# Kernel tuning notes

Measured on AMD Instinct MI355X. Metric: run time of the kernel, lower is better.

## Reference

```python
import jax, jax.numpy as jnp
import numpy as np

B, T, H, N = 4, 512, 32, 64
D = H * N  # n_embd = 2048


def setup_inputs() -> dict:
    key = jax.random.key(0)
    ks = jax.random.split(key, 8)
    f = lambda kk: jax.random.normal(kk, (B, T, H, N), dtype=jnp.float32)
    r = f(ks[0])
    w = f(ks[1])
    k = f(ks[2])
    v = f(ks[3])
    iclr = f(ks[4])
    # int8-style quantized output projection: int values in [-128,127] + per-row scale
    w_out_q = jax.random.randint(ks[5], (D, D), -128, 128, dtype=jnp.int32)
    w_out_scale = jax.random.uniform(ks[6], (D,), dtype=jnp.float32) * 0.01
    return {"r": r, "w": w, "k": k, "v": v, "iclr": iclr,
            "w_out_q": w_out_q, "w_out_scale": w_out_scale}


def _wkv7(r, w, k, v, iclr):
    """RWKV x070 WKV scan. All inputs [B,T,H,N]; returns [B,T,H*N]."""
    decay = jnp.exp(-jnp.exp(w))  # per-channel decay in (0,1), x070 parameterization
    # kk = l2-normalized key direction; a = -kk (removal), b = kk * sigmoid(iclr) (write)
    kk = k * jax.lax.rsqrt(jnp.sum(k * k, axis=-1, keepdims=True) + 1e-12)
    a = -kk
    b = kk * jax.nn.sigmoid(iclr)

    def step(state, inp):
        # state: [B,H,N,N]; each inp element: [B,H,N]
        r_t, d_t, k_t, v_t, a_t, b_t = inp
        sa = jnp.einsum('bhij,bhj->bhi', state, a_t)
        state = (state * d_t[:, :, None, :]
                 + sa[..., None] * b_t[:, :, None, :]
                 + v_t[..., None] * k_t[:, :, None, :])
        y_t = jnp.einsum('bhij,bhj->bhi', state, r_t)
        return state, y_t

    tb = lambda x: jnp.swapaxes(x, 0, 1)  # [B,T,H,N] -> [T,B,H,N]
    state0 = jnp.zeros((B, H, N, N), dtype=r.dtype)
    _, y = jax.lax.scan(step, state0, (tb(r), tb(decay), tb(k), tb(v), tb(a), tb(b)))
    return jnp.swapaxes(y, 0, 1).reshape(B, T, H * N)


def reference(r, w, k, v, iclr, w_out_q, w_out_scale):
    y = _wkv7(r, w, k, v, iclr)               # [B,T,D]
    # inline dequant of quantized output projection (per-output-row scale)
    W = w_out_q.astype(jnp.float32) * w_out_scale[:, None]  # [D,D]
    return jnp.einsum('btd,od->bto', y, W)    # [B,T,D]
```

## Files before the change

kernel.cpp:

```cpp
#include <hip/hip_runtime.h>
#include <hip/hip_bf16.h>
#include <stdint.h>

#define B_ 4
#define T_ 512
#define H_ 32
#define N_ 64
#define D_ 2048
#define M_ (B_*T_)

typedef __attribute__((ext_vector_type(4))) float f32x4;
typedef __attribute__((ext_vector_type(8))) short short8;

template <int CTRL>
__device__ __forceinline__ float dpp_add(float x) {
    int t = __builtin_amdgcn_mov_dpp(__float_as_int(x), CTRL, 0xF, 0xF, true);
    return x + __int_as_float(t);
}
__device__ __forceinline__ float bfly16(float x) {
    x = dpp_add<0xB1>(x);
    x = dpp_add<0x4E>(x);
    x = dpp_add<0x141>(x);
    x = dpp_add<0x140>(x);
    return x;
}

__device__ __forceinline__ void gld16(const float* g, float* l) {
    __builtin_amdgcn_global_load_lds(
        (const __attribute__((address_space(1))) unsigned int*)g,
        (__attribute__((address_space(3))) unsigned int*)l, 16, 0, 0);
}

__global__ __launch_bounds__(256) void prep(
    const float* __restrict__ r, const float* __restrict__ w,
    const float* __restrict__ k, const float* __restrict__ v,
    const float* __restrict__ iclr, float* __restrict__ pk) {
    int g = blockIdx.x * 4 + (threadIdx.x >> 6);
    int lane = threadIdx.x & 63;
    int b = g >> 14;
    int t = (g >> 5) & (T_ - 1);
    int h = g & 31;
    size_t si = (size_t)g * 64 + lane;
    size_t di = (((size_t)(b * H_ + h) * T_) + t) * 384 + lane;
    float rv = r[si], wv = w[si], kv = k[si], vv = v[si], av = iclr[si];
    float d = expf(-expf(wv));
    float ss = kv * kv;
#pragma unroll
    for (int m = 1; m < 64; m <<= 1) ss += __shfl_xor(ss, m, 64);
    float kkv = kv * rsqrtf(ss + 1e-12f);
    float bbv = kkv * (1.f / (1.f + expf(-av)));
    pk[di          ] = rv;
    pk[di + 1 * 64 ] = kv;
    pk[di + 2 * 64 ] = vv;
    pk[di + 3 * 64 ] = d;
    pk[di + 4 * 64 ] = kkv;
    pk[di + 5 * 64 ] = bbv;
}

__global__ __launch_bounds__(512) void wkv_scan(
    const float* __restrict__ pk, __hip_bfloat16* __restrict__ y,
    const int* __restrict__ q, __hip_bfloat16* __restrict__ o) {
    if (blockIdx.x >= 256) {
        int i = ((blockIdx.x - 256) * 512 + (int)threadIdx.x) * 4;
        int4 qi = *(const int4*)(q + i);
        __hip_bfloat16 t[4];
        t[0] = __float2bfloat16((float)qi.x);
        t[1] = __float2bfloat16((float)qi.y);
        t[2] = __float2bfloat16((float)qi.z);
        t[3] = __float2bfloat16((float)qi.w);
        *(uint2*)(o + i) = *(uint2*)t;
        return;
    }
    const int bh   = blockIdx.x & 127;
    const int half = blockIdx.x >> 7;
    const int tid  = threadIdx.x;
    const int wave = tid >> 6;
    const int lane = tid & 63;
    const int b = bh >> 5, h = bh & 31;
    const int jg = lane & 15;
    const int rl = lane >> 4;
    const int row = (half * 8 + wave) * 4 + rl;

    __shared__ __align__(16) float ring[2 * 1536];

    const float* src = pk + (size_t)bh * T_ * 384;

    if (wave == 0) {
#pragma unroll
        for (int gg = 0; gg < 2; ++gg)
#pragma unroll
            for (int c = 0; c < 6; ++c)
                gld16(src + gg * 1536 + c * 256 + lane * 4,
                      &ring[gg * 1536 + c * 256]);
    }

    float S[4] = {0.f, 0.f, 0.f, 0.f};

    for (int g = 0; g < T_ / 4; ++g) {
        if (wave == 0) {
            if (g == 0) { asm volatile("s_waitcnt vmcnt(6)"  ::: "memory"); }
            else        { asm volatile("s_waitcnt vmcnt(10)" ::: "memory"); }
        }
        asm volatile("s_barrier" ::: "memory");
        const float* rb0 = &ring[(g & 1) * 1536];

#pragma unroll
        for (int i = 0; i < 4; ++i) {
            const int t = g * 4 + i;
            const float* rb = rb0 + i * 384;

            f32x4 Rc = *(const f32x4*)(rb + 0 * 64 + jg * 4);
            f32x4 Kc = *(const f32x4*)(rb + 1 * 64 + jg * 4);
            float vcv =                 rb[2 * 64 + row];
            f32x4 Dc = *(const f32x4*)(rb + 3 * 64 + jg * 4);
            f32x4 Ac = *(const f32x4*)(rb + 4 * 64 + jg * 4);
            f32x4 Bc = *(const f32x4*)(rb + 5 * 64 + jg * 4);

            float s01 = fmaf(S[1], Ac[1], S[0] * Ac[0]);
            float s23 = fmaf(S[3], Ac[3], S[2] * Ac[2]);
            const float sa = -bfly16(s01 + s23);

            float t0 = fmaf(sa, Bc[0], vcv * Kc[0]);
            S[0] = fmaf(S[0], Dc[0], t0);
            float t1 = fmaf(sa, Bc[1], vcv * Kc[1]);
            S[1] = fmaf(S[1], Dc[1], t1);
            float y01 = fmaf(S[1], Rc[1], S[0] * Rc[0]);
            float t2 = fmaf(sa, Bc[2], vcv * Kc[2]);
            S[2] = fmaf(S[2], Dc[2], t2);
            float t3 = fmaf(sa, Bc[3], vcv * Kc[3]);
            S[3] = fmaf(S[3], Dc[3], t3);
            float y23 = fmaf(S[3], Rc[3], S[2] * Rc[2]);
            float ys = bfly16(y01 + y23);
            if (jg == 0)
                y[((size_t)b * T_ + t) * D_ + h * 64 + row] = __float2bfloat16(ys);
        }

        asm volatile("s_barrier" ::: "memory");

        if (wave == 0) {
            int gp = g + 2; if (gp > T_ / 4 - 1) gp = T_ / 4 - 1;
            const float* g0 = src + (size_t)gp * 1536 + lane * 4;
            float* l0 = &ring[(g & 1) * 1536];
#pragma unroll
            for (int c = 0; c < 6; ++c)
                gld16(g0 + c * 256, l0 + c * 256);
        }
    }
}

__device__ __forceinline__ void gload_lds16(const __hip_bfloat16* g, ushort* l) {
    __builtin_amdgcn_global_load_lds(
        (const __attribute__((address_space(1))) unsigned int*)g,
        (__attribute__((address_space(3))) unsigned int*)l, 16, 0, 0);
}

__global__ __launch_bounds__(256, 2) void gemm_bt(
    const __hip_bfloat16* __restrict__ A,
    const __hip_bfloat16* __restrict__ Bq,
    const float* __restrict__ scale,
    float* __restrict__ C) {
    const int K = D_;
    __shared__ __align__(16) ushort As[2][128 * 64];
    __shared__ __align__(16) ushort Bs[2][64 * 64];

    const int tid = threadIdx.x;
    const int lane = tid & 63;
    const int wave = tid >> 6;
    const int wr = wave >> 1, wc = wave & 1;

    const int id = blockIdx.x;
    const int swz = (id & 7) * 64 + (id >> 3);
    const int m0 = (swz & 15) * 128;
    const int n0 = (swz >> 4) * 64;

    const int srow8 = lane >> 3;
    const int scol8 = (lane & 7) * 8;
    const int ml = lane & 15;
    const int kq = (lane >> 4) * 8;

    f32x4 acc[4][2] = {};

#define GSTAGE(slot, kk0)                                                    \
    {                                                                        \
        _Pragma("unroll")                                                    \
        for (int c = 0; c < 4; ++c) {                                        \
            int ra = wave * 32 + c * 8;                                      \
            gload_lds16(A + (size_t)(m0 + ra + srow8) * K + (kk0) + scol8,   \
                        &As[slot][ra * 64]);                                 \
        }                                                                    \
        _Pragma("unroll")                                                    \
        for (int c = 0; c < 2; ++c) {                                        \
            int rb = wave * 16 + c * 8;                                      \
            gload_lds16(Bq + (size_t)(n0 + rb + srow8) * K + (kk0) + scol8,  \
                        &Bs[slot][rb * 64]);                                 \
        }                                                                    \
    }

    GSTAGE(0, 0);

    for (int t = 0; t < K / 64; ++t) {
        if (t + 1 < K / 64) {
            GSTAGE((t + 1) & 1, (t + 1) * 64);
            asm volatile("s_waitcnt vmcnt(6)" ::: "memory");
        } else {
            asm volatile("s_waitcnt vmcnt(0)" ::: "memory");
        }
        asm volatile("s_barrier" ::: "memory");
        const int sl = t & 1;
#pragma unroll
        for (int ks = 0; ks < 2; ++ks) {
            short8 af[4], bf[2];
#pragma unroll
            for (int tm = 0; tm < 4; ++tm)
                af[tm] = *(const short8*)(&As[sl][(wr * 64 + tm * 16 + ml) * 64 + ks * 32 + kq]);
#pragma unroll
            for (int tn = 0; tn < 2; ++tn)
                bf[tn] = *(const short8*)(&Bs[sl][(wc * 32 + tn * 16 + ml) * 64 + ks * 32 + kq]);
#pragma unroll
            for (int tm = 0; tm < 4; ++tm)
#pragma unroll
                for (int tn = 0; tn < 2; ++tn)
                    acc[tm][tn] = __builtin_amdgcn_mfma_f32_16x16x32_bf16(
                        af[tm], bf[tn], acc[tm][tn], 0, 0, 0);
        }
        asm volatile("s_barrier" ::: "memory");
    }
#undef GSTAGE

#pragma unroll
    for (int tn = 0; tn < 2; ++tn) {
        int gn = n0 + wc * 32 + tn * 16 + ml;
        float sc = scale[gn];
#pragma unroll
        for (int tm = 0; tm < 4; ++tm) {
            int gm = m0 + wr * 64 + tm * 16 + (lane >> 4) * 4;
#pragma unroll
            for (int rg = 0; rg < 4; ++rg)
                C[(size_t)(gm + rg) * D_ + gn] = acc[tm][tn][rg] * sc;
        }
    }
}

extern "C" void kernel_launch(void* const* d_in, const int* in_sizes, int n_in,
                              void* d_out, int out_size, void* d_ws, size_t ws_size,
                              hipStream_t stream) {
    (void)in_sizes; (void)n_in; (void)out_size; (void)ws_size;
    const float* r  = (const float*)d_in[0];
    const float* w  = (const float*)d_in[1];
    const float* k  = (const float*)d_in[2];
    const float* v  = (const float*)d_in[3];
    const float* ic = (const float*)d_in[4];
    const int*   wq = (const int*)d_in[5];
    const float* sc = (const float*)d_in[6];
    float* out = (float*)d_out;

    char* p = (char*)d_ws;
    __hip_bfloat16* yb = (__hip_bfloat16*)p;  p += (size_t)M_ * D_ * 2;
    __hip_bfloat16* wb = (__hip_bfloat16*)p;  p += (size_t)D_ * D_ * 2;
    float* pk = (float*)p;

    prep    <<<dim3(16384), dim3(256), 0, stream>>>(r, w, k, v, ic, pk);
    wkv_scan<<<dim3(256 + 2048), dim3(512), 0, stream>>>(pk, yb, wq, wb);
    gemm_bt <<<dim3(512), dim3(256), 0, stream>>>(yb, wb, sc, out);
}
```

Before: 287.8 us.

## Fuse prep into WKV scan and enlarge GEMM tile to 128x128

Removes the separate prep kernel and its packed workspace. The scan kernel now streams raw r/w/k/v/iclr rows into shared memory with 4-byte global-to-LDS loads and computes decay, normalized key and sigmoid gate inline using fast exp2/rcp/rsq intrinsics. This saves a kernel launch and a full write-then-read of the packed intermediate, but the serial scan loop now carries extra transcendental work and many more small load instructions. The GEMM also moves to 128x128 tiles with 256 blocks, which raises per-block reuse but halves the grid and drops the two-blocks-per-CU occupancy hint.

```diff
diff --git a/kernel.cpp b/kernel.cpp
--- a/kernel.cpp
+++ b/kernel.cpp
@@ -25,40 +25,16 @@
     return x;
 }
 
-__device__ __forceinline__ void gld16(const float* g, float* l) {
+__device__ __forceinline__ void gld4(const float* g, float* l) {
     __builtin_amdgcn_global_load_lds(
         (const __attribute__((address_space(1))) unsigned int*)g,
-        (__attribute__((address_space(3))) unsigned int*)l, 16, 0, 0);
-}
-
-__global__ __launch_bounds__(256) void prep(
+        (__attribute__((address_space(3))) unsigned int*)l, 4, 0, 0);
+}
+
+__global__ __launch_bounds__(512) void wkv_scan(
     const float* __restrict__ r, const float* __restrict__ w,
     const float* __restrict__ k, const float* __restrict__ v,
-    const float* __restrict__ iclr, float* __restrict__ pk) {
-    int g = blockIdx.x * 4 + (threadIdx.x >> 6);
-    int lane = threadIdx.x & 63;
-    int b = g >> 14;
-    int t = (g >> 5) & (T_ - 1);
-    int h = g & 31;
-    size_t si = (size_t)g * 64 + lane;
-    size_t di = (((size_t)(b * H_ + h) * T_) + t) * 384 + lane;
-    float rv = r[si], wv = w[si], kv = k[si], vv = v[si], av = iclr[si];
-    float d = expf(-expf(wv));
-    float ss = kv * kv;
-#pragma unroll
-    for (int m = 1; m < 64; m <<= 1) ss += __shfl_xor(ss, m, 64);
-    float kkv = kv * rsqrtf(ss + 1e-12f);
-    float bbv = kkv * (1.f / (1.f + expf(-av)));
-    pk[di          ] = rv;
-    pk[di + 1 * 64 ] = kv;
-    pk[di + 2 * 64 ] = vv;
-    pk[di + 3 * 64 ] = d;
-    pk[di + 4 * 64 ] = kkv;
-    pk[di + 5 * 64 ] = bbv;
-}
-
-__global__ __launch_bounds__(512) void wkv_scan(
-    const float* __restrict__ pk, __hip_bfloat16* __restrict__ y,
+    const float* __restrict__ iclr, __hip_bfloat16* __restrict__ y,
     const int* __restrict__ q, __hip_bfloat16* __restrict__ o) {
     if (blockIdx.x >= 256) {
         int i = ((blockIdx.x - 256) * 512 + (int)threadIdx.x) * 4;
@@ -81,40 +57,63 @@
     const int rl = lane >> 4;
     const int row = (half * 8 + wave) * 4 + rl;
 
-    __shared__ __align__(16) float ring[2 * 1536];
-
-    const float* src = pk + (size_t)bh * T_ * 384;
+    __shared__ __align__(16) float ring[2 * 1280];
+
+    const float L2E = 1.4426950408889634f;
 
     if (wave == 0) {
 #pragma unroll
         for (int gg = 0; gg < 2; ++gg)
 #pragma unroll
-            for (int c = 0; c < 6; ++c)
-                gld16(src + gg * 1536 + c * 256 + lane * 4,
-                      &ring[gg * 1536 + c * 256]);
+            for (int i = 0; i < 4; ++i) {
+                size_t base = ((size_t)(b * T_ + gg * 4 + i) * H_ + h) * 64 + lane;
+                float* l = &ring[gg * 1280 + i * 320];
+                gld4(r + base, l);
+                gld4(w + base, l + 64);
+                gld4(k + base, l + 128);
+                gld4(v + base, l + 192);
+                gld4(iclr + base, l + 256);
+            }
     }
 
     float S[4] = {0.f, 0.f, 0.f, 0.f};
 
     for (int g = 0; g < T_ / 4; ++g) {
         if (wave == 0) {
-            if (g == 0) { asm volatile("s_waitcnt vmcnt(6)"  ::: "memory"); }
-            else        { asm volatile("s_waitcnt vmcnt(10)" ::: "memory"); }
-        }
-        asm volatile("s_barrier" ::: "memory");
-        const float* rb0 = &ring[(g & 1) * 1536];
+            if (g == 0) { asm volatile("s_waitcnt vmcnt(20)" ::: "memory"); }
+            else        { asm volatile("s_waitcnt vmcnt(24)" ::: "memory"); }
+        }
+        asm volatile("s_barrier" ::: "memory");
+        const float* rb0 = &ring[(g & 1) * 1280];
 
 #pragma unroll
         for (int i = 0; i < 4; ++i) {
             const int t = g * 4 + i;
-            const float* rb = rb0 + i * 384;
-
-            f32x4 Rc = *(const f32x4*)(rb + 0 * 64 + jg * 4);
-            f32x4 Kc = *(const f32x4*)(rb + 1 * 64 + jg * 4);
-            float vcv =                 rb[2 * 64 + row];
-            f32x4 Dc = *(const f32x4*)(rb + 3 * 64 + jg * 4);
-            f32x4 Ac = *(const f32x4*)(rb + 4 * 64 + jg * 4);
-            f32x4 Bc = *(const f32x4*)(rb + 5 * 64 + jg * 4);
+            const float* rb = rb0 + i * 320;
+
+            f32x4 Rc = *(const f32x4*)(rb + jg * 4);
+            f32x4 Wc = *(const f32x4*)(rb + 64 + jg * 4);
+            f32x4 Kc = *(const f32x4*)(rb + 128 + jg * 4);
+            float vcv =                 rb[192 + row];
+            f32x4 Ic = *(const f32x4*)(rb + 256 + jg * 4);
+
+            float ss = Kc[0] * Kc[0];
+            ss = fmaf(Kc[1], Kc[1], ss);
+            ss = fmaf(Kc[2], Kc[2], ss);
+            ss = fmaf(Kc[3], Kc[3], ss);
+            ss = bfly16(ss);
+            float rs = __builtin_amdgcn_rsqf(ss + 1e-12f);
+            f32x4 Dc, Ac, Bc;
+#pragma unroll
+            for (int j = 0; j < 4; ++j) {
+                float e1 = __builtin_amdgcn_exp2f(Wc[j] * L2E);
+                Dc[j] = __builtin_amdgcn_exp2f(-e1 * L2E);
+                float kkv = Kc[j] * rs;
+                Ac[j] = kkv;
+                float sg = __builtin_amdgcn_rcpf(
+                    1.f + __builtin_amdgcn_exp2f(-Ic[j] * L2E));
+                Bc[j] = kkv * sg;
+            }
 
             float s01 = fmaf(S[1], Ac[1], S[0] * Ac[0]);
             float s23 = fmaf(S[3], Ac[3], S[2] * Ac[2]);
@@ -139,11 +138,17 @@
 
         if (wave == 0) {
             int gp = g + 2; if (gp > T_ / 4 - 1) gp = T_ / 4 - 1;
-            const float* g0 = src + (size_t)gp * 1536 + lane * 4;
-            float* l0 = &ring[(g & 1) * 1536];
-#pragma unroll
-            for (int c = 0; c < 6; ++c)
-                gld16(g0 + c * 256, l0 + c * 256);
+            float* l0 = &ring[(g & 1) * 1280];
+#pragma unroll
+            for (int i = 0; i < 4; ++i) {
+                size_t base = ((size_t)(b * T_ + gp * 4 + i) * H_ + h) * 64 + lane;
+                float* l = l0 + i * 320;
+                gld4(r + base, l);
+                gld4(w + base, l + 64);
+                gld4(k + base, l + 128);
+                gld4(v + base, l + 192);
+                gld4(iclr + base, l + 256);
+            }
         }
     }
 }
@@ -154,14 +159,14 @@
         (__attribute__((address_space(3))) unsigned int*)l, 16, 0, 0);
 }
 
-__global__ __launch_bounds__(256, 2) void gemm_bt(
+__global__ __launch_bounds__(256) void gemm_bt(
     const __hip_bfloat16* __restrict__ A,
     const __hip_bfloat16* __restrict__ Bq,
     const float* __restrict__ scale,
     float* __restrict__ C) {
     const int K = D_;
     __shared__ __align__(16) ushort As[2][128 * 64];
-    __shared__ __align__(16) ushort Bs[2][64 * 64];
+    __shared__ __align__(16) ushort Bs[2][128 * 64];
 
     const int tid = threadIdx.x;
     const int lane = tid & 63;
@@ -169,16 +174,16 @@
     const int wr = wave >> 1, wc = wave & 1;
 
     const int id = blockIdx.x;
-    const int swz = (id & 7) * 64 + (id >> 3);
+    const int swz = (id & 7) * 32 + (id >> 3);
     const int m0 = (swz & 15) * 128;
-    const int n0 = (swz >> 4) * 64;
+    const int n0 = (swz >> 4) * 128;
 
     const int srow8 = lane >> 3;
     const int scol8 = (lane & 7) * 8;
     const int ml = lane & 15;
     const int kq = (lane >> 4) * 8;
 
-    f32x4 acc[4][2] = {};
+    f32x4 acc[4][4] = {};
 
 #define GSTAGE(slot, kk0)                                                    \
     {                                                                        \
@@ -187,12 +192,8 @@
             int ra = wave * 32 + c * 8;                                      \
             gload_lds16(A + (size_t)(m0 + ra + srow8) * K + (kk0) + scol8,   \
                         &As[slot][ra * 64]);                                 \
-        }                                                                    \
-        _Pragma("unroll")                                                    \
-        for (int c = 0; c < 2; ++c) {                                        \
-            int rb = wave * 16 + c * 8;                                      \
-            gload_lds16(Bq + (size_t)(n0 + rb + srow8) * K + (kk0) + scol8,  \
-                        &Bs[slot][rb * 64]);                                 \
+            gload_lds16(Bq + (size_t)(n0 + ra + srow8) * K + (kk0) + scol8,  \
+                        &Bs[slot][ra * 64]);                                 \
         }                                                                    \
     }
 
@@ -201,7 +202,7 @@
     for (int t = 0; t < K / 64; ++t) {
         if (t + 1 < K / 64) {
             GSTAGE((t + 1) & 1, (t + 1) * 64);
-            asm volatile("s_waitcnt vmcnt(6)" ::: "memory");
+            asm volatile("s_waitcnt vmcnt(8)" ::: "memory");
         } else {
             asm volatile("s_waitcnt vmcnt(0)" ::: "memory");
         }
@@ -209,17 +210,17 @@
         const int sl = t & 1;
 #pragma unroll
         for (int ks = 0; ks < 2; ++ks) {
-            short8 af[4], bf[2];
+            short8 af[4], bf[4];
 #pragma unroll
             for (int tm = 0; tm < 4; ++tm)
                 af[tm] = *(const short8*)(&As[sl][(wr * 64 + tm * 16 + ml) * 64 + ks * 32 + kq]);
 #pragma unroll
-            for (int tn = 0; tn < 2; ++tn)
-                bf[tn] = *(const short8*)(&Bs[sl][(wc * 32 + tn * 16 + ml) * 64 + ks * 32 + kq]);
+            for (int tn = 0; tn < 4; ++tn)
+                bf[tn] = *(const short8*)(&Bs[sl][(wc * 64 + tn * 16 + ml) * 64 + ks * 32 + kq]);
 #pragma unroll
             for (int tm = 0; tm < 4; ++tm)
 #pragma unroll
-                for (int tn = 0; tn < 2; ++tn)
+                for (int tn = 0; tn < 4; ++tn)
                     acc[tm][tn] = __builtin_amdgcn_mfma_f32_16x16x32_bf16(
                         af[tm], bf[tn], acc[tm][tn], 0, 0, 0);
         }
@@ -228,8 +229,8 @@
 #undef GSTAGE
 
 #pragma unroll
-    for (int tn = 0; tn < 2; ++tn) {
-        int gn = n0 + wc * 32 + tn * 16 + ml;
+    for (int tn = 0; tn < 4; ++tn) {
+        int gn = n0 + wc * 64 + tn * 16 + ml;
         float sc = scale[gn];
 #pragma unroll
         for (int tm = 0; tm < 4; ++tm) {
@@ -256,10 +257,8 @@
 
     char* p = (char*)d_ws;
     __hip_bfloat16* yb = (__hip_bfloat16*)p;  p += (size_t)M_ * D_ * 2;
-    __hip_bfloat16* wb = (__hip_bfloat16*)p;  p += (size_t)D_ * D_ * 2;
-    float* pk = (float*)p;
-
-    prep    <<<dim3(16384), dim3(256), 0, stream>>>(r, w, k, v, ic, pk);
-    wkv_scan<<<dim3(256 + 2048), dim3(512), 0, stream>>>(pk, yb, wq, wb);
-    gemm_bt <<<dim3(512), dim3(256), 0, stream>>>(yb, wb, sc, out);
-}
+    __hip_bfloat16* wb = (__hip_bfloat16*)p;
+
+    wkv_scan<<<dim3(256 + 2048), dim3(512), 0, stream>>>(r, w, k, v, ic, yb, wq, wb);
+    gemm_bt <<<dim3(256), dim3(256), 0, stream>>>(yb, wb, sc, out);
+}
```

New measurement: 389.6 us. +35.4%, slower.
